# Kernel optimization log

Measured on AMD Instinct MI355X. Metric: run time of the kernel, lower is better.

Reference implementation:

```python
import jax, jax.numpy as jnp
import numpy as np

ALPHA = 16.0
R = 8.0
SCALE = ALPHA / R  # scaling = alpha / r, same for every adapter


def setup_inputs() -> dict:
    key = jax.random.key(0)
    ks = jax.random.split(key, 5)
    B_, S, D = 4, 2048, 4096
    E, r = 8, 8
    x = jax.random.normal(ks[0], (B_, S, D), dtype=jnp.float32)
    W = jax.random.normal(ks[1], (D, D), dtype=jnp.float32) * (1.0 / np.sqrt(D))
    b = jax.random.normal(ks[2], (D,), dtype=jnp.float32) * 0.02
    A = jax.random.normal(ks[3], (E, r, D), dtype=jnp.float32) * (1.0 / np.sqrt(D))
    Bm = jax.random.normal(ks[4], (E, D, r), dtype=jnp.float32) * 0.02
    return {"x": x, "W": W, "b": b, "A": A, "B": Bm}


def reference(x, W, b, A, B):
    # base = F.linear(x, W, b)
    base = jnp.einsum('bsi,oi->bso', x, W) + b
    # lora_total = sum_e scale * (x @ A_e.T @ B_e.T); all experts stacked.
    # intermediate [B,S,E,r] is tiny (r=8)
    t = jnp.einsum('bsi,eri->bser', x, A)
    lora = jnp.einsum('bser,eor->bso', t, B) * SCALE
    return base + lora
```

## Files before the change

kernel.cpp:

```cpp
#include <hip/hip_runtime.h>
#include <hip/hip_bf16.h>

typedef unsigned short u16;
typedef __bf16 bf16x8 __attribute__((ext_vector_type(8)));
typedef float f32x16 __attribute__((ext_vector_type(16)));

constexpr int Mdim = 8192;
constexpr int Ndim = 4096;
constexpr int Kdim = 4096;
constexpr int ER   = 64;
constexpr float LSCALE = 2.0f;

__device__ __forceinline__ u16 f2bf(float f) {
    union { float f; unsigned u; } v; v.f = f;
    unsigned r = v.u + 0x7fffu + ((v.u >> 16) & 1u);
    return (u16)(r >> 16);
}

#define GLOAD_LDS16(g, l)                                             \
    __builtin_amdgcn_global_load_lds(                                 \
        (const __attribute__((address_space(1))) void*)(g),           \
        (__attribute__((address_space(3))) void*)(l), 16, 0, 0)

__global__ __launch_bounds__(256) void weff_kernel(
    const float* __restrict__ W, const float* __restrict__ A,
    const float* __restrict__ Bm, u16* __restrict__ Wb)
{
    __shared__ __align__(16) float sAc[ER][128];
    __shared__ __align__(16) float sBc[64][ER];

    const int t  = threadIdx.x;
    const int i0 = blockIdx.x * 128;
    const int o0 = blockIdx.y * 64;

#pragma unroll
    for (int p = 0; p < 8; ++p) {
        int lin = p * 1024 + t * 4;
        int er = lin >> 7, ci = lin & 127;
        *(float4*)&sAc[er][ci] = *(const float4*)(A + (size_t)er * Kdim + i0 + ci);
    }
    {
        int ol = t >> 2;
        int c  = (t & 3) * 16;
#pragma unroll
        for (int q = 0; q < 2; ++q) {
            int er = c + q * 8;
            int e  = er >> 3;
            const float* src = Bm + ((size_t)e * Ndim + (o0 + ol)) * 8;
            *(float4*)&sBc[ol][er]     = *(const float4*)(src);
            *(float4*)&sBc[ol][er + 4] = *(const float4*)(src + 4);
        }
    }
    __syncthreads();

    const int tx = t & 31;
    const int ty = t >> 5;
    float acc[8][4] = {};
#pragma unroll 4
    for (int er = 0; er < ER; ++er) {
        float4 a = *(const float4*)&sAc[er][tx * 4];
#pragma unroll
        for (int q = 0; q < 8; ++q) {
            float bv = sBc[q * 8 + ty][er];
            acc[q][0] += bv * a.x;
            acc[q][1] += bv * a.y;
            acc[q][2] += bv * a.z;
            acc[q][3] += bv * a.w;
        }
    }
#pragma unroll
    for (int q = 0; q < 8; ++q) {
        int o = o0 + q * 8 + ty;
        const float4 w = *(const float4*)(W + (size_t)o * Kdim + i0 + tx * 4);
        ushort4 st;
        st.x = f2bf(w.x + LSCALE * acc[q][0]);
        st.y = f2bf(w.y + LSCALE * acc[q][1]);
        st.z = f2bf(w.z + LSCALE * acc[q][2]);
        st.w = f2bf(w.w + LSCALE * acc[q][3]);
        *(ushort4*)(Wb + (size_t)o * Kdim + i0 + tx * 4) = st;
    }
}

__global__ __launch_bounds__(256) void cvt_x_kernel(
    const float* __restrict__ x, u16* __restrict__ xb)
{
    size_t i = (size_t)blockIdx.x * blockDim.x + threadIdx.x;
    const float4 v0 = *(const float4*)(x + i * 8);
    const float4 v1 = *(const float4*)(x + i * 8 + 4);
    uint4 o;
    o.x = (unsigned)f2bf(v0.x) | ((unsigned)f2bf(v0.y) << 16);
    o.y = (unsigned)f2bf(v0.z) | ((unsigned)f2bf(v0.w) << 16);
    o.z = (unsigned)f2bf(v1.x) | ((unsigned)f2bf(v1.y) << 16);
    o.w = (unsigned)f2bf(v1.z) | ((unsigned)f2bf(v1.w) << 16);
    *(uint4*)(xb + i * 8) = o;
}

constexpr int BM = 256, BN = 256, BK = 64;
constexpr int NT = Kdim / BK;

__global__ __launch_bounds__(256, 1) void gemm_bias_kernel(
    const u16* __restrict__ Xb, const u16* __restrict__ Wb,
    const float* __restrict__ bias, float* __restrict__ C)
{
    __shared__ __align__(16) u16 lds[65536];

    const int t    = threadIdx.x;
    const int lane = t & 63;
    const int wv   = t >> 6;
    const int wr2  = wv >> 1;
    const int wc2  = wv & 1;

    const int wg  = blockIdx.x;
    const int xcd = wg & 7, lid = wg >> 3;
    const int mt  = (xcd & 1) * 16 + (lid >> 2);
    const int ntl = (xcd >> 1) * 4 + (lid & 3);
    const int bm  = mt * BM;
    const int bn  = ntl * BN;

    u16* b0 = lds;
    u16* b1 = lds + 32768;

    const u16* gSrc[16]; int dOff[16];
#pragma unroll
    for (int i = 0; i < 16; ++i) {
        const int isB = i >> 3;
        const int c   = (i & 7) * 256 + t;
        const int row = c >> 3;
        const int scl = ((c ^ (c >> 3)) & 7) * 8;
        gSrc[i] = (isB ? Wb + (size_t)(bn + row) * Kdim
                       : Xb + (size_t)(bm + row) * Kdim) + scl;
        dOff[i] = isB * 16384 + c * 8;
    }

    const int l31   = lane & 31;
    const int khalf = lane >> 5;
    const int key   = l31 & 7;
    int cpk[4];
#pragma unroll
    for (int ks = 0; ks < 4; ++ks)
        cpk[ks] = (((ks * 2 + khalf) ^ key) & 7) * 8;

    f32x16 acc[4][4];
#pragma unroll
    for (int i = 0; i < 4; ++i)
#pragma unroll
        for (int j = 0; j < 4; ++j)
            acc[i][j] = (f32x16)(0.0f);

    bf16x8 aP[4], bP[4];
    bf16x8 aQ[4], bQ[4];

#define DS_K(BUF, AR, BR, KS)                                                 \
    _Pragma("unroll")                                                         \
    for (int mi = 0; mi < 4; ++mi)                                            \
        AR[mi] = *(const bf16x8*)                                             \
            &(BUF)[(wr2 * 128 + mi * 32 + l31) * 64 + cpk[KS]];               \
    _Pragma("unroll")                                                         \
    for (int ni = 0; ni < 4; ++ni)                                            \
        BR[ni] = *(const bf16x8*)                                             \
            &(BUF)[16384 + (wc2 * 128 + ni * 32 + l31) * 64 + cpk[KS]];

#define MQ(AR, BR)                                                            \
    _Pragma("unroll")                                                         \
    for (int mi = 0; mi < 4; ++mi)                                            \
        _Pragma("unroll")                                                     \
        for (int ni = 0; ni < 4; ++ni)                                        \
            acc[mi][ni] = __builtin_amdgcn_mfma_f32_32x32x16_bf16(            \
                AR[mi], BR[ni], acc[mi][ni], 0, 0, 0);

#define FENCE asm volatile("" ::: "memory")
#define BAR   __builtin_amdgcn_s_barrier(); FENCE

#define TILE(CUR, NXT, FIRST, LAST)                                           \
    {                                                                         \
        asm volatile("s_waitcnt vmcnt(0) lgkmcnt(0)" ::: "memory");           \
        BAR;                                                                  \
        if (!(FIRST)) { MQ(aQ, bQ); }                                         \
        if (!(LAST)) {                                                        \
            _Pragma("unroll")                                                 \
            for (int i = 0; i < 16; ++i)                                      \
                GLOAD_LDS16(gSrc[i] + koff, (NXT) + dOff[i]);                 \
            koff += 64;                                                       \
        }                                                                     \
        DS_K(CUR, aP, bP, 0);                                                 \
        DS_K(CUR, aQ, bQ, 1);                                                 \
        MQ(aP, bP);                                                           \
        DS_K(CUR, aP, bP, 2);                                                 \
        MQ(aQ, bQ);                                                           \
        DS_K(CUR, aQ, bQ, 3);                                                 \
        MQ(aP, bP);                                                           \
    }

#pragma unroll
    for (int i = 0; i < 16; ++i) GLOAD_LDS16(gSrc[i], b0 + dOff[i]);

    int koff = 64;

    TILE(b0, b1, 1, 0);
#pragma unroll 1
    for (int t2 = 0; t2 < (NT - 2) / 2; ++t2) {
        TILE(b1, b0, 0, 0);
        TILE(b0, b1, 0, 0);
    }
    TILE(b1, b0, 0, 1);
    MQ(aQ, bQ);

#undef TILE
#undef MQ
#undef DS_K

#pragma unroll
    for (int ni = 0; ni < 4; ++ni) {
        const int col = bn + wc2 * 128 + ni * 32 + l31;
        const float bv = bias[col];
#pragma unroll
        for (int mi = 0; mi < 4; ++mi) {
            const int rbase = bm + wr2 * 128 + mi * 32 + khalf * 4;
#pragma unroll
            for (int rg = 0; rg < 16; ++rg) {
                const int row = rbase + (rg & 3) + 8 * (rg >> 2);
                C[(size_t)row * Ndim + col] = acc[mi][ni][rg] + bv;
            }
        }
    }
}

__global__ __launch_bounds__(256) void naive_row_kernel(
    const float* __restrict__ x, const float* __restrict__ W,
    const float* __restrict__ bias, const float* __restrict__ A,
    const float* __restrict__ Bm, float* __restrict__ out)
{
    __shared__ float sx[Kdim];
    __shared__ float st[ER];
    const int m = blockIdx.x;
    const float* xr = x + (size_t)m * Kdim;
    for (int i = threadIdx.x; i < Kdim; i += 256) sx[i] = xr[i];
    __syncthreads();
    if (threadIdx.x < ER) {
        const float* ar = A + (size_t)threadIdx.x * Kdim;
        float s = 0.f;
        for (int i = 0; i < Kdim; ++i) s += sx[i] * ar[i];
        st[threadIdx.x] = s;
    }
    __syncthreads();
    for (int o = threadIdx.x; o < Ndim; o += 256) {
        const float* wr = W + (size_t)o * Kdim;
        float s = bias[o];
        for (int i = 0; i < Kdim; ++i) s += sx[i] * wr[i];
        float l = 0.f;
        for (int e = 0; e < 8; ++e) {
            const float* bp = Bm + ((size_t)e * Ndim + o) * 8;
            for (int r = 0; r < 8; ++r) l += st[e * 8 + r] * bp[r];
        }
        out[(size_t)m * Ndim + o] = s + LSCALE * l;
    }
}

extern "C" void kernel_launch(void* const* d_in, const int* in_sizes, int n_in,
                              void* d_out, int out_size, void* d_ws, size_t ws_size,
                              hipStream_t stream)
{
    const float* x  = (const float*)d_in[0];
    const float* W  = (const float*)d_in[1];
    const float* b  = (const float*)d_in[2];
    const float* A  = (const float*)d_in[3];
    const float* Bm = (const float*)d_in[4];
    float* out = (float*)d_out;

    const size_t xb_bytes = (size_t)Mdim * Kdim * 2;
    const size_t wb_bytes = (size_t)Ndim * Kdim * 2;

    if (ws_size >= xb_bytes + wb_bytes) {
        u16* Xb = (u16*)d_ws;
        u16* Wb = (u16*)((char*)d_ws + xb_bytes);
        cvt_x_kernel<<<(Mdim * (size_t)Kdim) / 8 / 256, 256, 0, stream>>>(x, Xb);
        weff_kernel<<<dim3(Kdim / 128, Ndim / 64), 256, 0, stream>>>(W, A, Bm, Wb);
        gemm_bias_kernel<<<dim3((Mdim / BM) * (Ndim / BN)), 256, 0, stream>>>(Xb, Wb, b, out);
    } else {
        naive_row_kernel<<<Mdim, 256, 0, stream>>>(x, W, b, A, Bm, out);
    }
}
```

Measured before the change: 306.7 us.

## Switch GEMM to 16x16x32 MFMA with restructured LDS pipeline and setprio

Replaces the 32x32x16 bf16 MFMA tiling (4x4 tiles per wave) with 16x16x32 MFMA (8x8 tiles per wave), which changes the LDS read pattern to two K-halves per 64-wide tile. It also rewrites global-to-LDS address generation as base pointers plus fixed row strides instead of 16 precomputed pointers, reorders the tile body so LDS reads overlap the next tile's prefetch, and raises wave priority around MFMA bursts. The intent is fewer VGPRs spent on address arrays, better overlap of loads with MFMA, and a possibly more efficient instruction shape. The cost is 64 accumulators per wave and twice as many fragment registers, which raises register pressure.

```diff
diff --git a/kernel.cpp b/kernel.cpp
--- a/kernel.cpp
+++ b/kernel.cpp
@@ -3,7 +3,7 @@
 
 typedef unsigned short u16;
 typedef __bf16 bf16x8 __attribute__((ext_vector_type(8)));
-typedef float f32x16 __attribute__((ext_vector_type(16)));
+typedef float f32x4 __attribute__((ext_vector_type(4)));
 
 constexpr int Mdim = 8192;
 constexpr int Ndim = 4096;
@@ -120,53 +120,47 @@
     u16* b0 = lds;
     u16* b1 = lds + 32768;
 
-    const u16* gSrc[16]; int dOff[16];
-#pragma unroll
-    for (int i = 0; i < 16; ++i) {
-        const int isB = i >> 3;
-        const int c   = (i & 7) * 256 + t;
-        const int row = c >> 3;
-        const int scl = ((c ^ (c >> 3)) & 7) * 8;
-        gSrc[i] = (isB ? Wb + (size_t)(bn + row) * Kdim
-                       : Xb + (size_t)(bm + row) * Kdim) + scl;
-        dOff[i] = isB * 16384 + c * 8;
-    }
-
-    const int l31   = lane & 31;
-    const int khalf = lane >> 5;
-    const int key   = l31 & 7;
-    int cpk[4];
-#pragma unroll
-    for (int ks = 0; ks < 4; ++ks)
-        cpk[ks] = (((ks * 2 + khalf) ^ key) & 7) * 8;
-
-    f32x16 acc[4][4];
-#pragma unroll
-    for (int i = 0; i < 4; ++i)
-#pragma unroll
-        for (int j = 0; j < 4; ++j)
-            acc[i][j] = (f32x16)(0.0f);
-
-    bf16x8 aP[4], bP[4];
-    bf16x8 aQ[4], bQ[4];
-
-#define DS_K(BUF, AR, BR, KS)                                                 \
+    const int scl  = ((t ^ (t >> 3)) & 7) * 8;
+    const int rl   = t >> 3;
+    const u16* aBase = Xb + (size_t)(bm + rl) * Kdim + scl;
+    const u16* bBase = Wb + (size_t)(bn + rl) * Kdim + scl;
+    const int dA = t * 8;
+    const int dB = 16384 + t * 8;
+    constexpr int RSTEP = 32 * Kdim;
+
+    const int fr  = lane & 15;
+    const int cp0 = ((((lane >> 4)    ) ^ (lane & 7)) & 7) * 8;
+    const int cp1 = ((((lane >> 4) + 4) ^ (lane & 7)) & 7) * 8;
+
+    f32x4 acc[8][8];
+#pragma unroll
+    for (int i = 0; i < 8; ++i)
+#pragma unroll
+        for (int j = 0; j < 8; ++j)
+            acc[i][j] = f32x4{0.f, 0.f, 0.f, 0.f};
+
+    bf16x8 aP[8], bP[8];
+    bf16x8 aQ[8], bQ[8];
+
+#define DS_K(BUF, AR, BR, CP)                                                 \
     _Pragma("unroll")                                                         \
-    for (int mi = 0; mi < 4; ++mi)                                            \
+    for (int mi = 0; mi < 8; ++mi)                                            \
         AR[mi] = *(const bf16x8*)                                             \
-            &(BUF)[(wr2 * 128 + mi * 32 + l31) * 64 + cpk[KS]];               \
+            &(BUF)[(wr2 * 128 + mi * 16 + fr) * 64 + (CP)];                   \
     _Pragma("unroll")                                                         \
-    for (int ni = 0; ni < 4; ++ni)                                            \
+    for (int ni = 0; ni < 8; ++ni)                                            \
         BR[ni] = *(const bf16x8*)                                             \
-            &(BUF)[16384 + (wc2 * 128 + ni * 32 + l31) * 64 + cpk[KS]];
+            &(BUF)[16384 + (wc2 * 128 + ni * 16 + fr) * 64 + (CP)];
 
 #define MQ(AR, BR)                                                            \
+    __builtin_amdgcn_s_setprio(1);                                            \
     _Pragma("unroll")                                                         \
-    for (int mi = 0; mi < 4; ++mi)                                            \
+    for (int mi = 0; mi < 8; ++mi)                                            \
         _Pragma("unroll")                                                     \
-        for (int ni = 0; ni < 4; ++ni)                                        \
-            acc[mi][ni] = __builtin_amdgcn_mfma_f32_32x32x16_bf16(            \
-                AR[mi], BR[ni], acc[mi][ni], 0, 0, 0);
+        for (int ni = 0; ni < 8; ++ni)                                        \
+            acc[mi][ni] = __builtin_amdgcn_mfma_f32_16x16x32_bf16(            \
+                AR[mi], BR[ni], acc[mi][ni], 0, 0, 0);                        \
+    __builtin_amdgcn_s_setprio(0);
 
 #define FENCE asm volatile("" ::: "memory")
 #define BAR   __builtin_amdgcn_s_barrier(); FENCE
@@ -175,24 +169,27 @@
     {                                                                         \
         asm volatile("s_waitcnt vmcnt(0) lgkmcnt(0)" ::: "memory");           \
         BAR;                                                                  \
-        if (!(FIRST)) { MQ(aQ, bQ); }                                         \
+        DS_K(CUR, aP, bP, cp0);                                               \
         if (!(LAST)) {                                                        \
             _Pragma("unroll")                                                 \
-            for (int i = 0; i < 16; ++i)                                      \
-                GLOAD_LDS16(gSrc[i] + koff, (NXT) + dOff[i]);                 \
+            for (int j = 0; j < 8; ++j)                                       \
+                GLOAD_LDS16(aBase + koff + j * RSTEP, (NXT) + dA + j * 2048); \
+            _Pragma("unroll")                                                 \
+            for (int j = 0; j < 8; ++j)                                       \
+                GLOAD_LDS16(bBase + koff + j * RSTEP, (NXT) + dB + j * 2048); \
             koff += 64;                                                       \
         }                                                                     \
-        DS_K(CUR, aP, bP, 0);                                                 \
-        DS_K(CUR, aQ, bQ, 1);                                                 \
+        if (!(FIRST)) { MQ(aQ, bQ); }                                         \
         MQ(aP, bP);                                                           \
-        DS_K(CUR, aP, bP, 2);                                                 \
-        MQ(aQ, bQ);                                                           \
-        DS_K(CUR, aQ, bQ, 3);                                                 \
-        MQ(aP, bP);                                                           \
-    }
-
-#pragma unroll
-    for (int i = 0; i < 16; ++i) GLOAD_LDS16(gSrc[i], b0 + dOff[i]);
+        DS_K(CUR, aQ, bQ, cp1);                                               \
+    }
+
+#pragma unroll
+    for (int j = 0; j < 8; ++j)
+        GLOAD_LDS16(aBase + j * RSTEP, b0 + dA + j * 2048);
+#pragma unroll
+    for (int j = 0; j < 8; ++j)
+        GLOAD_LDS16(bBase + j * RSTEP, b0 + dB + j * 2048);
 
     int koff = 64;
 
@@ -210,17 +207,15 @@
 #undef DS_K
 
 #pragma unroll
-    for (int ni = 0; ni < 4; ++ni) {
-        const int col = bn + wc2 * 128 + ni * 32 + l31;
+    for (int ni = 0; ni < 8; ++ni) {
+        const int col = bn + wc2 * 128 + ni * 16 + (lane & 15);
         const float bv = bias[col];
 #pragma unroll
-        for (int mi = 0; mi < 4; ++mi) {
-            const int rbase = bm + wr2 * 128 + mi * 32 + khalf * 4;
-#pragma unroll
-            for (int rg = 0; rg < 16; ++rg) {
-                const int row = rbase + (rg & 3) + 8 * (rg >> 2);
-                C[(size_t)row * Ndim + col] = acc[mi][ni][rg] + bv;
-            }
+        for (int mi = 0; mi < 8; ++mi) {
+            const int rbase = bm + wr2 * 128 + mi * 16 + (lane >> 4) * 4;
+#pragma unroll
+            for (int j = 0; j < 4; ++j)
+                C[(size_t)(rbase + j) * Ndim + col] = acc[mi][ni][j] + bv;
         }
     }
 }
```

After: 298.7 us. 2.6% less time.
